# Kernel optimization log

Measured on AMD Instinct MI355X. Metric: run time of the kernel, lower is better.

Reference implementation:

```python
import jax, jax.numpy as jnp
import numpy as np

B, S, H = 2, 2048, 1024
NH, HD = 16, 64
ROPE_BASE = 10000.0


def setup_inputs() -> dict:
    key = jax.random.key(0)
    ks = jax.random.split(key, 8)
    sc = 1.0 / np.sqrt(H)
    return {
        "hidden_states": jax.random.normal(ks[0], (B, S, H), dtype=jnp.float32),
        "position_ids": jnp.arange(S, dtype=jnp.int64 if jax.config.jax_enable_x64 else jnp.int32)[None, :],
        "Wq": jax.random.normal(ks[1], (H, H), dtype=jnp.float32) * sc,
        "bq": jax.random.normal(ks[2], (H,), dtype=jnp.float32) * 0.02,
        "Wk": jax.random.normal(ks[3], (H, H), dtype=jnp.float32) * sc,
        "bk": jax.random.normal(ks[4], (H,), dtype=jnp.float32) * 0.02,
        "Wv": jax.random.normal(ks[5], (H, H), dtype=jnp.float32) * sc,
        "bv": jax.random.normal(ks[6], (H,), dtype=jnp.float32) * 0.02,
        "Wo": jax.random.normal(ks[7], (H, H), dtype=jnp.float32) * sc,
    }


def _rotate_half(x):
    x1, x2 = x[..., : HD // 2], x[..., HD // 2:]
    return jnp.concatenate((-x2, x1), axis=-1)


def _rope_tables(seq_len, dtype):
    inv_freq = 1.0 / (ROPE_BASE ** (jnp.arange(0, HD, 2, dtype=jnp.float32) / HD))
    t = jnp.arange(seq_len, dtype=jnp.float32)
    freqs = jnp.einsum("s,d->sd", t, inv_freq)          # [S, HD/2]
    emb = jnp.concatenate((freqs, freqs), axis=-1)       # [S, HD]
    return jnp.cos(emb).astype(dtype), jnp.sin(emb).astype(dtype)


def reference(hidden_states, position_ids, Wq, bq, Wk, bk, Wv, bv, Wo):
    bsz, q_len, _ = hidden_states.shape
    # QKV projections (torch Linear: x @ W.T + b)
    q = (hidden_states @ Wq.T + bq).reshape(bsz, q_len, NH, HD).transpose(0, 2, 1, 3)
    k = (hidden_states @ Wk.T + bk).reshape(bsz, q_len, NH, HD).transpose(0, 2, 1, 3)
    v = (hidden_states @ Wv.T + bv).reshape(bsz, q_len, NH, HD).transpose(0, 2, 1, 3)
    # RoPE
    cos, sin = _rope_tables(q_len, hidden_states.dtype)
    cos = cos[position_ids][:, None]  # [1, 1, S, HD] (unsqueeze_dim=1)
    sin = sin[position_ids][:, None]
    q = q * cos + _rotate_half(q) * sin
    k = k * cos + _rotate_half(k) * sin
    # scaled dot-product attention (mask=None, dropout=0)
    scale = 1.0 / jnp.sqrt(jnp.asarray(HD, hidden_states.dtype))
    scores = jnp.einsum("bhqd,bhkd->bhqk", q, k) * scale
    probs = jax.nn.softmax(scores, axis=-1)
    attn = jnp.einsum("bhqk,bhkd->bhqd", probs, v)
    attn = attn.transpose(0, 2, 1, 3).reshape(bsz, q_len, H)
    return attn @ Wo.T
```

## Files before the change

### kernel.cpp

```cpp
#include <hip/hip_runtime.h>
#include <hip/hip_bf16.h>
#include <math.h>

#define SS 2048
#define HH 1024
#define NHH 16
#define HDD 64
#define BH 32
#define MM 4096

typedef unsigned short u16;
using bf16x8 = __attribute__((ext_vector_type(8))) short;
using floatx4 = __attribute__((ext_vector_type(4))) float;

__device__ __forceinline__ u16 f2bf(float f) {
  unsigned u = __float_as_uint(f);
  u += 0x7fffu + ((u >> 16) & 1u);
  return (u16)(u >> 16);
}
__device__ __forceinline__ unsigned pk_bf16(float a, float b) {
  union { __hip_bfloat162 h2; unsigned u; } c;
  c.h2 = __float22bfloat162_rn(float2{a, b});
  return c.u;
}
__device__ __forceinline__ void gload_lds16(const u16* g, u16* l) {
  __builtin_amdgcn_global_load_lds(
      (const __attribute__((address_space(1))) void*)g,
      (__attribute__((address_space(3))) void*)l, 16, 0, 0);
}

__global__ __launch_bounds__(256) void convert_bf(
    const float* __restrict__ hs, const float* __restrict__ wq,
    const float* __restrict__ wk, const float* __restrict__ wv,
    const float* __restrict__ wo, const int* __restrict__ pos,
    u16* __restrict__ hs_b, u16* __restrict__ wq_b, u16* __restrict__ wk_b,
    u16* __restrict__ wv_b, u16* __restrict__ wo_b,
    float2* __restrict__ tab) {
  int g = blockIdx.x * 256 + threadIdx.x;
  if (g < 2097152) {
    const float* src;
    u16* dst;
    int off;
    if (g < 1048576) {
      src = hs; dst = hs_b; off = g;
    } else {
      int t = g - 1048576;
      int w = t >> 18;
      off = t & 262143;
      src = (w == 0) ? wq : (w == 1) ? wk : (w == 2) ? wv : wo;
      dst = (w == 0) ? wq_b : (w == 1) ? wk_b : (w == 2) ? wv_b : wo_b;
    }
    float4 v = ((const float4*)src)[off];
    ushort4 o = make_ushort4(f2bf(v.x), f2bf(v.y), f2bf(v.z), f2bf(v.w));
    ((ushort4*)dst)[off] = o;
  } else {
    int idx = g - 2097152;
    int s = idx >> 5, j = idx & 31;
    float p = (float)pos[s];
    const float c0 = 13.287712379549449f / 32.0f;
    float f = p * exp2f(-(float)j * c0);
    float sn, cs;
    sincosf(f, &sn, &cs);
    tab[idx] = float2{cs, sn};
  }
}

__global__ __launch_bounds__(256) void mfma_gemm_qkv(
    const u16* __restrict__ X, const u16* __restrict__ W0,
    const u16* __restrict__ W1, const u16* __restrict__ W2,
    const float* __restrict__ b0, const float* __restrict__ b1,
    const float* __restrict__ b2, const float2* __restrict__ tab,
    u16* __restrict__ O0, u16* __restrict__ O1, u16* __restrict__ O2) {
  __shared__ __align__(16) u16 As[128 * 32];
  __shared__ __align__(16) u16 Bs[128 * 32];
  const int tid = threadIdx.x;
  const int lane = tid & 63;
  const int wvu = __builtin_amdgcn_readfirstlane(tid >> 6);
  const int l15 = lane & 15;
  const int quad = lane >> 4;
  const int wm = wvu >> 1, wn = wvu & 1;
  const int m0 = blockIdx.y * 128;
  const int n0g = blockIdx.x * 128;
  const int lr = lane >> 2;
  const int lc = lane & 3;

  int wsel = n0g >> 10;
  int n0 = n0g & 1023;
  const u16* Wsel = (wsel == 1) ? W1 : (wsel == 2) ? W2 : W0;
  const float* bsel = (wsel == 1) ? b1 : (wsel == 2) ? b2 : b0;
  u16* Osel = (wsel == 1) ? O1 : (wsel == 2) ? O2 : O0;

  floatx4 acc[4][4];
#pragma unroll
  for (int i = 0; i < 4; ++i)
#pragma unroll
    for (int j = 0; j < 4; ++j) acc[i][j] = (floatx4){0.f, 0.f, 0.f, 0.f};

  const int scol = (lc ^ ((lr >> 1) & 3)) * 8;
  const int fsw = ((l15 >> 1) & 3);

  for (int k0 = 0; k0 < HH; k0 += 32) {
#pragma unroll
    for (int u = 0; u < 2; ++u) {
      int r = u * 64 + wvu * 16 + lr;
      gload_lds16(&X[(size_t)(m0 + r) * HH + k0 + scol],
                  &As[(u * 64 + wvu * 16) * 32]);
      gload_lds16(&Wsel[(size_t)(n0 + r) * HH + k0 + scol],
                  &Bs[(u * 64 + wvu * 16) * 32]);
    }
    __syncthreads();
    bf16x8 af[4], bfr[4];
#pragma unroll
    for (int mb = 0; mb < 4; ++mb)
      af[mb] = *(const bf16x8*)&As[(wm * 64 + mb * 16 + l15) * 32 +
                                   ((quad ^ fsw) * 8)];
#pragma unroll
    for (int nb = 0; nb < 4; ++nb)
      bfr[nb] = *(const bf16x8*)&Bs[(wn * 64 + nb * 16 + l15) * 32 +
                                    ((quad ^ fsw) * 8)];
#pragma unroll
    for (int mb = 0; mb < 4; ++mb)
#pragma unroll
      for (int nb = 0; nb < 4; ++nb)
        acc[mb][nb] = __builtin_amdgcn_mfma_f32_16x16x32_bf16(
            af[mb], bfr[nb], acc[mb][nb], 0, 0, 0);
    __syncthreads();
  }

  if (wsel < 2) {
    const float qs = (wsel == 0) ? 0.125f * 1.44269504088896f : 1.0f;
    const int colb = n0 + wn * 64;
    const int h = colb >> 6;
    const float bias0 = bsel[colb + l15];
    const float bias1 = bsel[colb + 16 + l15];
    const float bias2 = bsel[colb + 32 + l15];
    const float bias3 = bsel[colb + 48 + l15];
#pragma unroll
    for (int mb = 0; mb < 4; ++mb)
#pragma unroll
      for (int r = 0; r < 4; ++r) {
        int m = m0 + wm * 64 + mb * 16 + quad * 4 + r;
        int b = m >> 11, s = m & (SS - 1);
        float2 t0 = tab[s * 32 + l15];
        float2 t1 = tab[s * 32 + 16 + l15];
        size_t obase = ((size_t)(b * NHH + h) * SS + s) * HDD;
        float x1 = acc[mb][0][r] + bias0;
        float x2 = acc[mb][2][r] + bias2;
        Osel[obase + l15] = f2bf((x1 * t0.x - x2 * t0.y) * qs);
        Osel[obase + 32 + l15] = f2bf((x2 * t0.x + x1 * t0.y) * qs);
        float y1 = acc[mb][1][r] + bias1;
        float y2 = acc[mb][3][r] + bias3;
        Osel[obase + 16 + l15] = f2bf((y1 * t1.x - y2 * t1.y) * qs);
        Osel[obase + 48 + l15] = f2bf((y2 * t1.x + y1 * t1.y) * qs);
      }
  } else {
#pragma unroll
    for (int nb = 0; nb < 4; ++nb) {
      int col = n0 + wn * 64 + nb * 16 + l15;
      int h = col >> 6, d = col & 63;
      float bias = bsel[col];
#pragma unroll
      for (int mb = 0; mb < 4; ++mb) {
        int m = m0 + wm * 64 + mb * 16 + quad * 4;
        int b = m >> 11, s = m & (SS - 1);
        uint2 w2;
        w2.x = pk_bf16(acc[mb][nb][0] + bias, acc[mb][nb][1] + bias);
        w2.y = pk_bf16(acc[mb][nb][2] + bias, acc[mb][nb][3] + bias);
        *(uint2*)&Osel[((size_t)((b * NHH + h) * HDD + d)) * SS + s] = w2;
      }
    }
  }
}

__global__ __launch_bounds__(256) void gemm_out(const u16* __restrict__ X,
                                                const u16* __restrict__ W,
                                                float* __restrict__ Ofp) {
  __shared__ __align__(16) u16 As[128 * 32];
  __shared__ __align__(16) u16 Bs[64 * 32];
  const int tid = threadIdx.x;
  const int lane = tid & 63;
  const int wvu = __builtin_amdgcn_readfirstlane(tid >> 6);
  const int l15 = lane & 15;
  const int quad = lane >> 4;
  const int wm = wvu >> 1, wn = wvu & 1;
  const int m0 = blockIdx.y * 128;
  const int n0 = blockIdx.x * 64;
  const int lr = lane >> 2;
  const int lc = lane & 3;

  floatx4 acc[4][2];
#pragma unroll
  for (int i = 0; i < 4; ++i)
#pragma unroll
    for (int j = 0; j < 2; ++j) acc[i][j] = (floatx4){0.f, 0.f, 0.f, 0.f};

  const int scol = (lc ^ ((lr >> 1) & 3)) * 8;
  const int fsw = ((l15 >> 1) & 3);

  for (int k0 = 0; k0 < HH; k0 += 32) {
#pragma unroll
    for (int u = 0; u < 2; ++u) {
      int r = u * 64 + wvu * 16 + lr;
      gload_lds16(&X[(size_t)(m0 + r) * HH + k0 + scol],
                  &As[(u * 64 + wvu * 16) * 32]);
    }
    gload_lds16(&W[(size_t)(n0 + wvu * 16 + lr) * HH + k0 + scol],
                &Bs[(wvu * 16) * 32]);
    __syncthreads();
    bf16x8 af[4], bfr[2];
#pragma unroll
    for (int mb = 0; mb < 4; ++mb)
      af[mb] = *(const bf16x8*)&As[(wm * 64 + mb * 16 + l15) * 32 +
                                   ((quad ^ fsw) * 8)];
#pragma unroll
    for (int nb = 0; nb < 2; ++nb)
      bfr[nb] = *(const bf16x8*)&Bs[(wn * 32 + nb * 16 + l15) * 32 +
                                    ((quad ^ fsw) * 8)];
#pragma unroll
    for (int mb = 0; mb < 4; ++mb)
#pragma unroll
      for (int nb = 0; nb < 2; ++nb)
        acc[mb][nb] = __builtin_amdgcn_mfma_f32_16x16x32_bf16(
            af[mb], bfr[nb], acc[mb][nb], 0, 0, 0);
    __syncthreads();
  }

#pragma unroll
  for (int mb = 0; mb < 4; ++mb)
#pragma unroll
    for (int r = 0; r < 4; ++r) {
      int m = m0 + wm * 64 + mb * 16 + quad * 4 + r;
#pragma unroll
      for (int nb = 0; nb < 2; ++nb)
        Ofp[(size_t)m * HH + n0 + wn * 32 + nb * 16 + l15] = acc[mb][nb][r];
    }
}

__global__ __launch_bounds__(256, 4) void attn_mfma(const u16* __restrict__ Qg,
                                                    const u16* __restrict__ Kg,
                                                    const u16* __restrict__ Vtg,
                                                    u16* __restrict__ A) {
  __shared__ __align__(16) u16 smem[16384];
  u16* const Ks0 = smem;
  u16* const Ks1 = smem + 4096;
  u16* const Vs0 = smem + 8192;
  u16* const Vs1 = smem + 12288;
  float* const lpart = (float*)smem;
  float* const Opart = (float*)smem + 128;

  const int tid = threadIdx.x;
  const int lane = tid & 63;
  const int wv = __builtin_amdgcn_readfirstlane(tid >> 6);
  const int l15 = lane & 15, quad = lane >> 4;
  const int sw7 = l15 & 7;
  const int bh = blockIdx.x, qt = blockIdx.y;
  const size_t hb = (size_t)bh * SS * HDD;
  const int kh = wv >> 1;
  const int qh = wv & 1;

  const int r8 = lane >> 3, c7 = lane & 7;
  const int cs = (c7 ^ r8) * 8;
  const u16* kgb[2];
  const u16* vgb[2];
#pragma unroll
  for (int u = 0; u < 2; ++u) {
    int row = (wv * 2 + u) * 8 + r8;
    kgb[u] = Kg + hb + (size_t)row * HDD + cs;
    vgb[u] = Vtg + hb + (size_t)row * SS + cs;
  }

#pragma unroll
  for (int u = 0; u < 2; ++u) {
    int row = (wv * 2 + u) * 8 + r8;
    gload_lds16(&Qg[hb + (size_t)(qt * 64 + row) * HDD + cs],
                Ks1 + (wv * 2 + u) * 512);
    gload_lds16(kgb[u], Ks0 + (wv * 2 + u) * 512);
    gload_lds16(vgb[u], Vs0 + (wv * 2 + u) * 512);
  }
  __syncthreads();

  bf16x8 qf[2][2];
#pragma unroll
  for (int nb = 0; nb < 2; ++nb)
#pragma unroll
    for (int h2 = 0; h2 < 2; ++h2)
      qf[nb][h2] = *(const bf16x8*)&Ks1[(qh * 32 + nb * 16 + l15) * 64 +
                                        (((h2 * 4 + quad) ^ sw7) * 8)];
  __syncthreads();

  float l_acc[2] = {0.f, 0.f};
  floatx4 o[4][2];
#pragma unroll
  for (int dmb = 0; dmb < 4; ++dmb)
#pragma unroll
    for (int nb = 0; nb < 2; ++nb) o[dmb][nb] = (floatx4){0.f, 0.f, 0.f, 0.f};

  const u16* kp[2];
  const u16* vp[2];
#pragma unroll
  for (int u = 0; u < 2; ++u) {
    kp[u] = kgb[u] + 64 * HDD;
    vp[u] = vgb[u] + 64;
  }

  auto tile_compute = [&](const u16* ks, const u16* vs) {
    floatx4 st[2][2];
    __builtin_amdgcn_s_setprio(1);
#pragma unroll
    for (int kmb = 0; kmb < 2; ++kmb) {
      int krow = kh * 32 + kmb * 16 + l15;
      bf16x8 ak0 = *(const bf16x8*)&ks[krow * 64 + ((quad ^ sw7) * 8)];
      bf16x8 ak1 = *(const bf16x8*)&ks[krow * 64 + (((4 + quad) ^ sw7) * 8)];
#pragma unroll
      for (int nb = 0; nb < 2; ++nb) {
        floatx4 z = (floatx4){0.f, 0.f, 0.f, 0.f};
        z = __builtin_amdgcn_mfma_f32_16x16x32_bf16(ak0, qf[nb][0], z, 0, 0, 0);
        z = __builtin_amdgcn_mfma_f32_16x16x32_bf16(ak1, qf[nb][1], z, 0, 0, 0);
        st[kmb][nb] = z;
      }
    }
    __builtin_amdgcn_s_setprio(0);

    bf16x8 bp[2];
#pragma unroll
    for (int nb = 0; nb < 2; ++nb) {
      float p00 = __builtin_amdgcn_exp2f(st[0][nb][0]);
      float p01 = __builtin_amdgcn_exp2f(st[0][nb][1]);
      float p02 = __builtin_amdgcn_exp2f(st[0][nb][2]);
      float p03 = __builtin_amdgcn_exp2f(st[0][nb][3]);
      float p10 = __builtin_amdgcn_exp2f(st[1][nb][0]);
      float p11 = __builtin_amdgcn_exp2f(st[1][nb][1]);
      float p12 = __builtin_amdgcn_exp2f(st[1][nb][2]);
      float p13 = __builtin_amdgcn_exp2f(st[1][nb][3]);
      l_acc[nb] += ((p00 + p01) + (p02 + p03)) + ((p10 + p11) + (p12 + p13));
      union { bf16x8 v; unsigned u[4]; } pu;
      pu.u[0] = pk_bf16(p00, p01);
      pu.u[1] = pk_bf16(p02, p03);
      pu.u[2] = pk_bf16(p10, p11);
      pu.u[3] = pk_bf16(p12, p13);
      bp[nb] = pu.v;
    }

    const int cb0 = kh * 4 + (quad >> 1);
    const int cb1 = cb0 + 2;
    const int sub = (quad & 1) * 4;
    __builtin_amdgcn_s_setprio(1);
#pragma unroll
    for (int dmb = 0; dmb < 4; ++dmb) {
      int vr = (dmb * 16 + l15) * 64;
      union { bf16x8 v; uint2 d2[2]; } au;
      au.d2[0] = *(const uint2*)&vs[vr + ((cb0 ^ sw7) * 8) + sub];
      au.d2[1] = *(const uint2*)&vs[vr + ((cb1 ^ sw7) * 8) + sub];
#pragma unroll
      for (int nb = 0; nb < 2; ++nb)
        o[dmb][nb] = __builtin_amdgcn_mfma_f32_16x16x32_bf16(au.v, bp[nb],
                                                             o[dmb][nb], 0, 0, 0);
    }
    __builtin_amdgcn_s_setprio(0);
  };

  for (int tt = 0; tt < SS / 64; tt += 2) {
#pragma unroll
    for (int u = 0; u < 2; ++u) {
      gload_lds16(kp[u], Ks1 + (wv * 2 + u) * 512);
      gload_lds16(vp[u], Vs1 + (wv * 2 + u) * 512);
      kp[u] += 64 * HDD;
      vp[u] += 64;
    }
    tile_compute(Ks0, Vs0);
    __syncthreads();

    if (tt < SS / 64 - 2) {
#pragma unroll
      for (int u = 0; u < 2; ++u) {
        gload_lds16(kp[u], Ks0 + (wv * 2 + u) * 512);
        gload_lds16(vp[u], Vs0 + (wv * 2 + u) * 512);
      }
    }
#pragma unroll
    for (int u = 0; u < 2; ++u) {
      kp[u] += 64 * HDD;
      vp[u] += 64;
    }
    tile_compute(Ks1, Vs1);
    __syncthreads();
  }

#pragma unroll
  for (int nb = 0; nb < 2; ++nb) {
    l_acc[nb] += __shfl_xor(l_acc[nb], 16);
    l_acc[nb] += __shfl_xor(l_acc[nb], 32);
  }
  if (quad == 0) {
    lpart[wv * 32 + l15] = l_acc[0];
    lpart[wv * 32 + 16 + l15] = l_acc[1];
  }
  if (kh == 1) {
    float* dst = Opart + qh * (32 * 68);
#pragma unroll
    for (int nb = 0; nb < 2; ++nb)
#pragma unroll
      for (int dmb = 0; dmb < 4; ++dmb)
        *(floatx4*)&dst[(nb * 16 + l15) * 68 + dmb * 16 + quad * 4] =
            o[dmb][nb];
  }
  __syncthreads();
  if (kh == 0) {
    const int b = bh >> 4, h = bh & 15;
    const float* src = Opart + qh * (32 * 68);
    float inv[2];
#pragma unroll
    for (int nb = 0; nb < 2; ++nb)
      inv[nb] = 1.f / (lpart[wv * 32 + nb * 16 + l15] +
                       lpart[(wv + 2) * 32 + nb * 16 + l15]);
#pragma unroll
    for (int nb = 0; nb < 2; ++nb) {
      int s = qt * 64 + qh * 32 + nb * 16 + l15;
#pragma unroll
      for (int dmb = 0; dmb < 4; ++dmb) {
        floatx4 part =
            *(const floatx4*)&src[(nb * 16 + l15) * 68 + dmb * 16 + quad * 4];
        floatx4 tot = (o[dmb][nb] + part) * inv[nb];
        uint2 w2;
        w2.x = pk_bf16(tot[0], tot[1]);
        w2.y = pk_bf16(tot[2], tot[3]);
        *(uint2*)&A[((size_t)(b * SS + s) * HH) + h * HDD + dmb * 16 +
                    quad * 4] = w2;
      }
    }
  }
}

extern "C" void kernel_launch(void* const* d_in, const int* in_sizes, int n_in,
                              void* d_out, int out_size, void* d_ws,
                              size_t ws_size, hipStream_t stream) {
  const float* hs = (const float*)d_in[0];
  const int* pos = (const int*)d_in[1];
  const float* Wq = (const float*)d_in[2];
  const float* bq = (const float*)d_in[3];
  const float* Wk = (const float*)d_in[4];
  const float* bk = (const float*)d_in[5];
  const float* Wv = (const float*)d_in[6];
  const float* bv = (const float*)d_in[7];
  const float* Wo = (const float*)d_in[8];
  float* out = (float*)d_out;

  u16* hs_b = (u16*)d_ws;
  u16* wq_b = hs_b + 4194304;
  u16* wk_b = wq_b + 1048576;
  u16* wv_b = wk_b + 1048576;
  u16* wo_b = wv_b + 1048576;
  u16* Qb = wo_b + 1048576;
  u16* Kb = Qb + 4194304;
  u16* Vtb = Kb + 4194304;
  u16* Ab = Vtb + 4194304;
  float2* tab = (float2*)(Ab + 4194304);

  hipLaunchKernelGGL(convert_bf, dim3(8448), dim3(256), 0, stream, hs, Wq, Wk,
                     Wv, Wo, pos, hs_b, wq_b, wk_b, wv_b, wo_b, tab);
  hipLaunchKernelGGL(mfma_gemm_qkv, dim3(24, 32), dim3(256), 0, stream, hs_b,
                     wq_b, wk_b, wv_b, bq, bk, bv, tab, Qb, Kb, Vtb);
  hipLaunchKernelGGL(attn_mfma, dim3(32, 32), dim3(256), 0, stream, Qb, Kb,
                     Vtb, Ab);
  hipLaunchKernelGGL(gemm_out, dim3(16, 32), dim3(256), 0, stream, Ab, wo_b,
                     out);
}
```

Measured before the change: 201.1 us.

## Rewrite QKV GEMM with 256x256 tiles and double-buffered pipelined LDS staging

The fused QKV projection GEMM moves from 128x128 tiles with 256 threads to 256x256 tiles with 512 threads. It double-buffers a K=64 slice in LDS and overlaps asynchronous global-to-LDS loads with MFMA sub-phases, using barriers and raised wave priority around the MFMA work. A workgroup index swizzle is added to improve L2 reuse. The goal is to hide global load latency and raise data reuse per tile. The cost is fewer workgroups (192) than CUs, plus high register and LDS pressure.

After: 191.4 us. -4.8%, faster.

```diff
diff --git a/kernel.cpp b/kernel.cpp
--- a/kernel.cpp
+++ b/kernel.cpp
@@ -65,67 +65,165 @@
   }
 }
 
-__global__ __launch_bounds__(256) void mfma_gemm_qkv(
+__global__ __launch_bounds__(512, 2) void mfma_gemm_qkv(
     const u16* __restrict__ X, const u16* __restrict__ W0,
     const u16* __restrict__ W1, const u16* __restrict__ W2,
     const float* __restrict__ b0, const float* __restrict__ b1,
     const float* __restrict__ b2, const float2* __restrict__ tab,
     u16* __restrict__ O0, u16* __restrict__ O1, u16* __restrict__ O2) {
-  __shared__ __align__(16) u16 As[128 * 32];
-  __shared__ __align__(16) u16 Bs[128 * 32];
+  __shared__ __align__(16) u16 lds[65536];
   const int tid = threadIdx.x;
   const int lane = tid & 63;
-  const int wvu = __builtin_amdgcn_readfirstlane(tid >> 6);
-  const int l15 = lane & 15;
-  const int quad = lane >> 4;
-  const int wm = wvu >> 1, wn = wvu & 1;
-  const int m0 = blockIdx.y * 128;
-  const int n0g = blockIdx.x * 128;
-  const int lr = lane >> 2;
-  const int lc = lane & 3;
-
-  int wsel = n0g >> 10;
-  int n0 = n0g & 1023;
+  const int wv = __builtin_amdgcn_readfirstlane(tid >> 6);
+  const int l15 = lane & 15, quad = lane >> 4;
+  const int sw7 = l15 & 7;
+  const int wm = wv >> 2, wn = wv & 3;
+  const int r8 = lane >> 3, c7 = lane & 7;
+
+  int wg = blockIdx.x;
+  int swz = (wg & 7) * 24 + (wg >> 3);
+  int bx = swz % 12, by = swz / 12;
+  const int m0 = by * 256;
+  const int n0g = bx * 256;
+  const int wsel = n0g >> 10;
+  const int n0 = n0g & 1023;
   const u16* Wsel = (wsel == 1) ? W1 : (wsel == 2) ? W2 : W0;
   const float* bsel = (wsel == 1) ? b1 : (wsel == 2) ? b2 : b0;
   u16* Osel = (wsel == 1) ? O1 : (wsel == 2) ? O2 : O0;
 
-  floatx4 acc[4][4];
-#pragma unroll
-  for (int i = 0; i < 4; ++i)
+  u16* const ldsA = lds;
+  u16* const ldsB = lds + 32768;
+
+  const int csw = (c7 ^ r8) * 8;
+  const int rA0 = (wv >> 2) * 128 + (wv & 3) * 16;
+  const int rB0 = (wv >> 1) * 64 + (wv & 1) * 16;
+  const u16* gA0a = X + (size_t)(m0 + rA0 + r8) * HH + csw;
+  const u16* gA0b = gA0a + 8 * HH;
+  const u16* gA2a = gA0a + 64 * HH;
+  const u16* gA2b = gA0a + 72 * HH;
+  const u16* gB0a = Wsel + (size_t)(n0 + rB0 + r8) * HH + csw;
+  const u16* gB0b = gB0a + 8 * HH;
+  const u16* gB1a = gB0a + 32 * HH;
+  const u16* gB1b = gB0a + 40 * HH;
+  const int dA0 = rA0 * 64;
+  const int dA2 = dA0 + 4096;
+  const int dB0 = rB0 * 64;
+  const int dB1 = dB0 + 2048;
+
+#define STAGEU(pa, pb, base, doff, buf)                  \
+  do {                                                   \
+    u16* d_ = (base) + (buf) * 16384 + (doff);           \
+    gload_lds16((pa), d_);                               \
+    gload_lds16((pb), d_ + 512);                         \
+  } while (0)
+
+  floatx4 acc[8][4];
+#pragma unroll
+  for (int i = 0; i < 8; ++i)
 #pragma unroll
     for (int j = 0; j < 4; ++j) acc[i][j] = (floatx4){0.f, 0.f, 0.f, 0.f};
 
-  const int scol = (lc ^ ((lr >> 1) & 3)) * 8;
-  const int fsw = ((l15 >> 1) & 3);
-
-  for (int k0 = 0; k0 < HH; k0 += 32) {
-#pragma unroll
-    for (int u = 0; u < 2; ++u) {
-      int r = u * 64 + wvu * 16 + lr;
-      gload_lds16(&X[(size_t)(m0 + r) * HH + k0 + scol],
-                  &As[(u * 64 + wvu * 16) * 32]);
-      gload_lds16(&Wsel[(size_t)(n0 + r) * HH + k0 + scol],
-                  &Bs[(u * 64 + wvu * 16) * 32]);
-    }
-    __syncthreads();
-    bf16x8 af[4], bfr[4];
-#pragma unroll
-    for (int mb = 0; mb < 4; ++mb)
-      af[mb] = *(const bf16x8*)&As[(wm * 64 + mb * 16 + l15) * 32 +
-                                   ((quad ^ fsw) * 8)];
-#pragma unroll
-    for (int nb = 0; nb < 4; ++nb)
-      bfr[nb] = *(const bf16x8*)&Bs[(wn * 64 + nb * 16 + l15) * 32 +
-                                    ((quad ^ fsw) * 8)];
-#pragma unroll
-    for (int mb = 0; mb < 4; ++mb)
-#pragma unroll
-      for (int nb = 0; nb < 4; ++nb)
-        acc[mb][nb] = __builtin_amdgcn_mfma_f32_16x16x32_bf16(
-            af[mb], bfr[nb], acc[mb][nb], 0, 0, 0);
-    __syncthreads();
-  }
+  STAGEU(gA0a, gA0b, ldsA, dA0, 0);
+  STAGEU(gA2a, gA2b, ldsA, dA2, 0);
+  STAGEU(gB0a, gB0b, ldsB, dB0, 0);
+  STAGEU(gB1a, gB1b, ldsB, dB1, 0);
+  STAGEU(gA0a + 64, gA0b + 64, ldsA, dA0, 1);
+  STAGEU(gB0a + 64, gB0b + 64, ldsB, dB0, 1);
+  STAGEU(gA2a + 64, gA2b + 64, ldsA, dA2, 1);
+  asm volatile("s_waitcnt vmcnt(6)" ::: "memory");
+  __builtin_amdgcn_s_barrier();
+
+  const u16 *pUB1a = gB1a + 64, *pUB1b = gB1b + 64;
+  const u16 *pUA0a = gA0a + 128, *pUA0b = gA0b + 128;
+  const u16 *pUB0a = gB0a + 128, *pUB0b = gB0b + 128;
+  const u16 *pUA2a = gA2a + 128, *pUA2b = gA2b + 128;
+
+  bf16x8 af[4][2], bf0[2][2], bf1[2][2];
+
+#define LOADA(Ab, hm)                                                     \
+  _Pragma("unroll") for (int mb = 0; mb < 4; ++mb) {                      \
+    const u16* rp_ = (Ab) + (wm * 128 + (hm) * 64 + mb * 16 + l15) * 64;  \
+    af[mb][0] = *(const bf16x8*)&rp_[((quad ^ sw7) * 8)];                 \
+    af[mb][1] = *(const bf16x8*)&rp_[(((4 + quad) ^ sw7) * 8)];           \
+  }
+#define LOADB(dst, Bb, hn)                                                \
+  _Pragma("unroll") for (int nq = 0; nq < 2; ++nq) {                      \
+    const u16* rp_ = (Bb) + (wn * 64 + (hn) * 32 + nq * 16 + l15) * 64;   \
+    dst[nq][0] = *(const bf16x8*)&rp_[((quad ^ sw7) * 8)];                \
+    dst[nq][1] = *(const bf16x8*)&rp_[(((4 + quad) ^ sw7) * 8)];          \
+  }
+#define MFMAQ(bfh, hm, hn)                                                \
+  _Pragma("unroll") for (int mb = 0; mb < 4; ++mb)                        \
+  _Pragma("unroll") for (int nq = 0; nq < 2; ++nq) {                      \
+    acc[(hm) * 4 + mb][(hn) * 2 + nq] =                                   \
+        __builtin_amdgcn_mfma_f32_16x16x32_bf16(                          \
+            af[mb][0], bfh[nq][0], acc[(hm) * 4 + mb][(hn) * 2 + nq], 0,  \
+            0, 0);                                                        \
+    acc[(hm) * 4 + mb][(hn) * 2 + nq] =                                   \
+        __builtin_amdgcn_mfma_f32_16x16x32_bf16(                          \
+            af[mb][1], bfh[nq][1], acc[(hm) * 4 + mb][(hn) * 2 + nq], 0,  \
+            0, 0);                                                        \
+  }
+
+#pragma unroll 2
+  for (int t = 0; t < 16; ++t) {
+    const u16* Ac = ldsA + (t & 1) * 16384;
+    const u16* Bc = ldsB + (t & 1) * 16384;
+    const int nb1 = (t + 1) & 1;
+    const int nb2 = t & 1;
+    LOADA(Ac, 0);
+    LOADB(bf0, Bc, 0);
+    if (t < 15) {
+      STAGEU(pUB1a, pUB1b, ldsB, dB1, nb1);
+      pUB1a += 64; pUB1b += 64;
+    }
+    __builtin_amdgcn_s_barrier();
+    asm volatile("s_waitcnt lgkmcnt(0)" ::: "memory");
+    __builtin_amdgcn_s_setprio(1);
+    MFMAQ(bf0, 0, 0);
+    __builtin_amdgcn_s_setprio(0);
+    __builtin_amdgcn_s_barrier();
+    LOADB(bf1, Bc, 1);
+    if (t < 14) {
+      STAGEU(pUA0a, pUA0b, ldsA, dA0, nb2);
+      pUA0a += 64; pUA0b += 64;
+    }
+    __builtin_amdgcn_s_barrier();
+    asm volatile("s_waitcnt lgkmcnt(0)" ::: "memory");
+    __builtin_amdgcn_s_setprio(1);
+    MFMAQ(bf1, 0, 1);
+    __builtin_amdgcn_s_setprio(0);
+    __builtin_amdgcn_s_barrier();
+    LOADA(Ac, 1);
+    if (t < 14) {
+      STAGEU(pUB0a, pUB0b, ldsB, dB0, nb2);
+      pUB0a += 64; pUB0b += 64;
+    }
+    __builtin_amdgcn_s_barrier();
+    asm volatile("s_waitcnt lgkmcnt(0)" ::: "memory");
+    __builtin_amdgcn_s_setprio(1);
+    MFMAQ(bf0, 1, 0);
+    __builtin_amdgcn_s_setprio(0);
+    __builtin_amdgcn_s_barrier();
+    if (t < 14) {
+      STAGEU(pUA2a, pUA2b, ldsA, dA2, nb2);
+      pUA2a += 64; pUA2b += 64;
+    }
+    __builtin_amdgcn_s_setprio(1);
+    MFMAQ(bf1, 1, 1);
+    __builtin_amdgcn_s_setprio(0);
+    if (t < 14) {
+      asm volatile("s_waitcnt vmcnt(6)" ::: "memory");
+      __builtin_amdgcn_s_barrier();
+    } else if (t == 14) {
+      asm volatile("s_waitcnt vmcnt(0)" ::: "memory");
+      __builtin_amdgcn_s_barrier();
+    }
+  }
+#undef STAGEU
+#undef LOADA
+#undef LOADB
+#undef MFMAQ
 
   if (wsel < 2) {
     const float qs = (wsel == 0) ? 0.125f * 1.44269504088896f : 1.0f;
@@ -136,10 +234,10 @@
     const float bias2 = bsel[colb + 32 + l15];
     const float bias3 = bsel[colb + 48 + l15];
 #pragma unroll
-    for (int mb = 0; mb < 4; ++mb)
+    for (int mb = 0; mb < 8; ++mb)
 #pragma unroll
       for (int r = 0; r < 4; ++r) {
-        int m = m0 + wm * 64 + mb * 16 + quad * 4 + r;
+        int m = m0 + wm * 128 + mb * 16 + quad * 4 + r;
         int b = m >> 11, s = m & (SS - 1);
         float2 t0 = tab[s * 32 + l15];
         float2 t1 = tab[s * 32 + 16 + l15];
@@ -160,8 +258,8 @@
       int h = col >> 6, d = col & 63;
       float bias = bsel[col];
 #pragma unroll
-      for (int mb = 0; mb < 4; ++mb) {
-        int m = m0 + wm * 64 + mb * 16 + quad * 4;
+      for (int mb = 0; mb < 8; ++mb) {
+        int m = m0 + wm * 128 + mb * 16 + quad * 4;
         int b = m >> 11, s = m & (SS - 1);
         uint2 w2;
         w2.x = pk_bf16(acc[mb][nb][0] + bias, acc[mb][nb][1] + bias);
@@ -458,7 +556,7 @@
 
   hipLaunchKernelGGL(convert_bf, dim3(8448), dim3(256), 0, stream, hs, Wq, Wk,
                      Wv, Wo, pos, hs_b, wq_b, wk_b, wv_b, wo_b, tab);
-  hipLaunchKernelGGL(mfma_gemm_qkv, dim3(24, 32), dim3(256), 0, stream, hs_b,
+  hipLaunchKernelGGL(mfma_gemm_qkv, dim3(192), dim3(512), 0, stream, hs_b,
                      wq_b, wk_b, wv_b, bq, bk, bv, tab, Qb, Kb, Vtb);
   hipLaunchKernelGGL(attn_mfma, dim3(32, 32), dim3(256), 0, stream, Qb, Kb,
                      Vtb, Ab);
```
